# Performance work log

Measured on AMD Instinct MI355X. Metric: run time of the kernel, lower is better.

The kernel has to match this reference:

```python
import jax, jax.numpy as jnp
import numpy as np

DIMS = [2, 100, 100, 100, 98, 100, 100, 100, 100, 1]
BETA = 100.0

def _softplus100(x):
    # PyTorch Softplus(beta=100): (1/beta)*log(1+exp(beta*x)), linear above threshold 20
    bx = BETA * x
    return jnp.where(bx > 20.0, x, jax.nn.softplus(bx) / BETA)

def setup_inputs() -> dict:
    key = jax.random.key(0)
    keys = jax.random.split(key, 1 + 2 * 9)
    N = 1048576
    inp = {"input": jax.random.normal(keys[0], (N, 2), dtype=jnp.float32)}
    for l in range(9):
        in_dim = DIMS[l + 1] if l == 4 else DIMS[l]  # layer 4 is Linear(dims[5], dims[5]) = 100->100
        out_dim = DIMS[l + 1]
        # torch Linear convention: weight [out, in]
        scale = np.sqrt(2.0) / np.sqrt(out_dim)
        inp[f"W{l}"] = jax.random.normal(keys[1 + 2 * l], (out_dim, in_dim), dtype=jnp.float32) * scale
        inp[f"b{l}"] = jax.random.normal(keys[2 + 2 * l], (out_dim,), dtype=jnp.float32) * 0.01
    return inp

def reference(input, W0, b0, W1, b1, W2, b2, W3, b3, W4, b4, W5, b5, W6, b6, W7, b7, W8, b8):
    Ws = [W0, W1, W2, W3, W4, W5, W6, W7, W8]
    bs = [b0, b1, b2, b3, b4, b5, b6, b7, b8]
    x = input
    skip_input = input
    for l in range(9):
        if l == 4:
            x = jnp.concatenate([skip_input, x], axis=1)  # [N, 2+98] -> [N,100]
        x = x @ Ws[l].T + bs[l]
        if l < 8:
            x = _softplus100(x)
    return x  # [N, 1]
```

## Files before the change

### kernel.cpp

```cpp
#include <hip/hip_runtime.h>
#include <math.h>


typedef _Float16 half8 __attribute__((ext_vector_type(8)));
typedef _Float16 half4v __attribute__((ext_vector_type(4)));
typedef float f32x4 __attribute__((ext_vector_type(4)));

#define TPB 256
#define RPB 128

__device__ __forceinline__ float sp100(float x) {
    float t = __builtin_amdgcn_exp2f(-144.26950408889634f * fabsf(x));
    return fmaxf(x, 0.0f) + 0.0069314718055994531f * __builtin_amdgcn_logf(1.0f + t);
}

__device__ __forceinline__ int xhb(int m, int k) {
    return ((m << 8) + (k << 1)) ^ ((m & 7) << 4);
}

__global__ __launch_bounds__(TPB, 2) void mlp_fwd(
    const float* __restrict__ inp,
    const uint4* __restrict__ wpk,
    const float* __restrict__ W0, const float* __restrict__ b0,
    const float* __restrict__ W8, const float* __restrict__ b8,
    float* __restrict__ out)
{
    __shared__ _Float16 XH[RPB * 128];
    __shared__ _Float16 XL[RPB * 128];
    __shared__ float inps[RPB * 2];
    __shared__ float w0s[304];

    const int tid  = threadIdx.x;
    const int lane = tid & 63;
    const int wid  = tid >> 6;
    const int g    = lane >> 4;
    const int bid  = blockIdx.x;

    if (tid < RPB) {
        float2 v = *reinterpret_cast<const float2*>(inp + ((size_t)bid * RPB + tid) * 2);
        inps[tid * 2]     = v.x;
        inps[tid * 2 + 1] = v.y;
    }
    for (int q = tid; q < 304; q += TPB)
        w0s[q] = (q < 200) ? W0[q] : b0[q - 200];
    __syncthreads();

#pragma unroll
    for (int it = 0; it < 16; ++it) {
        int m = wid * 32 + it * 2 + (lane >> 5);
        int q = lane & 31;
        float i0 = inps[m * 2], i1 = inps[m * 2 + 1];
        half4v hh, hl;
#pragma unroll
        for (int p = 0; p < 4; ++p) {
            int c = q * 4 + p;
            float y = (c < 100)
                ? sp100(fmaf(i0, w0s[c * 2], fmaf(i1, w0s[c * 2 + 1], w0s[200 + c])))
                : ((c == 100) ? 1.0f : 0.0f);
            _Float16 h = (_Float16)y;
            hh[p] = h;
            hl[p] = (_Float16)(y - (float)h);
        }
        *reinterpret_cast<half4v*>(reinterpret_cast<char*>(XH) + xhb(m, q * 4)) = hh;
        *reinterpret_cast<half4v*>(reinterpret_cast<char*>(XL) + xhb(m, q * 4)) = hl;
    }

#pragma unroll 1
    for (int l = 1; l <= 7; ++l) {
        const uint4* __restrict__ wl = wpk + (size_t)(l - 1) * 3584;

        f32x4 acc[2][7];
#pragma unroll
        for (int rt = 0; rt < 2; ++rt)
#pragma unroll
            for (int t = 0; t < 7; ++t) acc[rt][t] = f32x4{0.f, 0.f, 0.f, 0.f};

#pragma unroll
        for (int s = 0; s < 4; ++s) {
            half8 Bh[2], Bl[2];
#pragma unroll
            for (int rt = 0; rt < 2; ++rt) {
                int m  = wid * 32 + rt * 16 + (lane & 15);
                int k0 = s * 32 + g * 8;
                Bh[rt] = *reinterpret_cast<const half8*>(
                             reinterpret_cast<const char*>(XH) + xhb(m, k0));
                Bl[rt] = *reinterpret_cast<const half8*>(
                             reinterpret_cast<const char*>(XL) + xhb(m, k0));
            }
#pragma unroll
            for (int t = 0; t < 7; ++t) {
                union { uint4 v; half8 h; } wh, wlo;
                wh.v  = wl[(s * 7 + t) * 64 + lane];
                wlo.v = wl[1792 + (s * 7 + t) * 64 + lane];
#pragma unroll
                for (int rt = 0; rt < 2; ++rt) {
                    acc[rt][t] = __builtin_amdgcn_mfma_f32_16x16x32_f16(wh.h,  Bh[rt], acc[rt][t], 0, 0, 0);
                    acc[rt][t] = __builtin_amdgcn_mfma_f32_16x16x32_f16(wh.h,  Bl[rt], acc[rt][t], 0, 0, 0);
                    acc[rt][t] = __builtin_amdgcn_mfma_f32_16x16x32_f16(wlo.h, Bh[rt], acc[rt][t], 0, 0, 0);
                }
            }
        }

        if (l < 7) {
            const int Nl = (l == 3) ? 98 : 100;
#pragma unroll
            for (int rt = 0; rt < 2; ++rt) {
                int m = wid * 32 + rt * 16 + (lane & 15);
#pragma unroll
                for (int t = 0; t < 7; ++t) {
                    half4v hh, hl;
#pragma unroll
                    for (int i = 0; i < 4; ++i) {
                        int n = 16 * t + 4 * g + i;
                        float y = (n < Nl) ? sp100(acc[rt][t][i])
                                           : ((n == Nl) ? 1.0f : 0.0f);
                        _Float16 h = (_Float16)y;
                        hh[i] = h;
                        hl[i] = (_Float16)(y - (float)h);
                    }
                    if (l != 3) {
                        *reinterpret_cast<half4v*>(
                            reinterpret_cast<char*>(XH) + xhb(m, 16 * t + 4 * g)) = hh;
                        *reinterpret_cast<half4v*>(
                            reinterpret_cast<char*>(XL) + xhb(m, 16 * t + 4 * g)) = hl;
                    } else {
#pragma unroll
                        for (int i = 0; i < 4; ++i) {
                            int c = 16 * t + 4 * g + i + 2;
                            *reinterpret_cast<_Float16*>(
                                reinterpret_cast<char*>(XH) + xhb(m, c)) = hh[i];
                            *reinterpret_cast<_Float16*>(
                                reinterpret_cast<char*>(XL) + xhb(m, c)) = hl[i];
                        }
                    }
                }
            }
            if (l == 3 && lane < 32) {
                int m = wid * 32 + lane;
#pragma unroll
                for (int c = 0; c < 2; ++c) {
                    float v = inps[m * 2 + c];
                    _Float16 h = (_Float16)v;
                    *reinterpret_cast<_Float16*>(
                        reinterpret_cast<char*>(XH) + xhb(m, c)) = h;
                    *reinterpret_cast<_Float16*>(
                        reinterpret_cast<char*>(XL) + xhb(m, c)) = (_Float16)(v - (float)h);
                }
            }
        } else {
            float w84[7][4];
#pragma unroll
            for (int t = 0; t < 6; ++t) {
                float4 w4 = *reinterpret_cast<const float4*>(W8 + 16 * t + 4 * g);
                w84[t][0] = w4.x; w84[t][1] = w4.y; w84[t][2] = w4.z; w84[t][3] = w4.w;
            }
#pragma unroll
            for (int i = 0; i < 4; ++i) {
                int n = 96 + 4 * g + i;
                w84[6][i] = (n < 100) ? W8[n] : 0.0f;
            }
            float p8[2] = {0.0f, 0.0f};
#pragma unroll
            for (int rt = 0; rt < 2; ++rt)
#pragma unroll
                for (int t = 0; t < 7; ++t)
#pragma unroll
                    for (int i = 0; i < 4; ++i)
                        p8[rt] = fmaf(w84[t][i], sp100(acc[rt][t][i]), p8[rt]);
            float b8v = b8[0];
#pragma unroll
            for (int rt = 0; rt < 2; ++rt) {
                float v = p8[rt];
                v += __shfl_xor(v, 16);
                v += __shfl_xor(v, 32);
                if (lane < 16)
                    out[(size_t)bid * RPB + wid * 32 + rt * 16 + lane] = v + b8v;
            }
        }
    }
}

__global__ void pack_weights(
    const float* __restrict__ W1, const float* __restrict__ W2,
    const float* __restrict__ W3, const float* __restrict__ W4,
    const float* __restrict__ W5, const float* __restrict__ W6,
    const float* __restrict__ W7,
    const float* __restrict__ b1, const float* __restrict__ b2,
    const float* __restrict__ b3, const float* __restrict__ b4,
    const float* __restrict__ b5, const float* __restrict__ b6,
    const float* __restrict__ b7,
    uint4* __restrict__ wpk)
{
    const float* Wt[7] = {W1, W2, W3, W4, W5, W6, W7};
    const float* Bt[7] = {b1, b2, b3, b4, b5, b6, b7};
    const float* W = Wt[blockIdx.x];
    const float* B = Bt[blockIdx.x];
    const int Nl = (blockIdx.x == 2) ? 98 : 100;
    for (int e = threadIdx.x; e < 3584; e += 256) {
        int term = e / 1792;
        int r    = e - term * 1792;
        int lane = r & 63;
        int st   = r >> 6;
        int s    = st / 7;
        int t    = st - s * 7;
        union { _Float16 h[8]; uint4 v; } pk;
#pragma unroll
        for (int jj = 0; jj < 8; ++jj) {
            int k = s * 32 + (lane >> 4) * 8 + jj;
            int n = t * 16 + (lane & 15);
            float val = 0.0f;
            if (n < Nl) {
                if (k < 100)       val = W[n * 100 + k];
                else if (k == 100) val = B[n];
            }
            _Float16 h = (_Float16)val;
            pk.h[jj] = term ? (_Float16)(val - (float)h) : h;
        }
        wpk[blockIdx.x * 3584 + term * 1792 + r] = pk.v;
    }
}

extern "C" void kernel_launch(void* const* d_in, const int* in_sizes, int n_in,
                              void* d_out, int out_size, void* d_ws, size_t ws_size,
                              hipStream_t stream)
{
    const float* inp = (const float*)d_in[0];
    const float* W[9];
    const float* B[9];
    for (int l = 0; l < 9; ++l) {
        W[l] = (const float*)d_in[1 + 2 * l];
        B[l] = (const float*)d_in[2 + 2 * l];
    }
    uint4* wpk = (uint4*)d_ws;
    float* out = (float*)d_out;
    const int N = in_sizes[0] / 2;

    pack_weights<<<7, 256, 0, stream>>>(W[1], W[2], W[3], W[4], W[5], W[6], W[7],
                                        B[1], B[2], B[3], B[4], B[5], B[6], B[7],
                                        wpk);
    mlp_fwd<<<N / RPB, TPB, 0, stream>>>(inp, wpk,
                                         W[0], B[0], W[8], B[8],
                                         out);
}
```

Baseline: 769.4 us.

## Double-buffer weight and activation fragments across K-steps and layers

Prefetches the next K-step's packed weight fragments (from global) and activation fragments (from LDS) into a second register buffer while the current step's MFMAs run. It also prefetches the next layer's first weight slice during the last step, and reorders the MFMAs so that independent accumulators are interleaved instead of chained three deep. The aim is to hide global and LDS load latency behind matrix work. The cost is many more live vector registers: two buffers of 14 weight half8 plus activations, on top of 14 accumulators. With launch bounds of 2 waves per SIMD, this risks spills or fewer resident waves.

After: 856.2 us. +11.3%, slower.

```diff
diff --git a/kernel.cpp b/kernel.cpp
--- a/kernel.cpp
+++ b/kernel.cpp
@@ -65,9 +65,28 @@
         *reinterpret_cast<half4v*>(reinterpret_cast<char*>(XL) + xhb(m, q * 4)) = hl;
     }
 
+    half8 wb[2][2][7];
+    half8 xb[2][2][2];
+
+    const half8* __restrict__ w8p = reinterpret_cast<const half8*>(wpk);
+
+#pragma unroll
+    for (int t = 0; t < 7; ++t) {
+        wb[0][0][t] = w8p[t * 64 + lane];
+        wb[0][1][t] = w8p[1792 + t * 64 + lane];
+    }
+#pragma unroll
+    for (int rt = 0; rt < 2; ++rt) {
+        int m = wid * 32 + rt * 16 + (lane & 15);
+        xb[0][0][rt] = *reinterpret_cast<const half8*>(
+                           reinterpret_cast<const char*>(XH) + xhb(m, g * 8));
+        xb[0][1][rt] = *reinterpret_cast<const half8*>(
+                           reinterpret_cast<const char*>(XL) + xhb(m, g * 8));
+    }
+
 #pragma unroll 1
     for (int l = 1; l <= 7; ++l) {
-        const uint4* __restrict__ wl = wpk + (size_t)(l - 1) * 3584;
+        const half8* __restrict__ wl = w8p + (size_t)(l - 1) * 3584;
 
         f32x4 acc[2][7];
 #pragma unroll
@@ -77,28 +96,50 @@
 
 #pragma unroll
         for (int s = 0; s < 4; ++s) {
-            half8 Bh[2], Bl[2];
-#pragma unroll
-            for (int rt = 0; rt < 2; ++rt) {
-                int m  = wid * 32 + rt * 16 + (lane & 15);
-                int k0 = s * 32 + g * 8;
-                Bh[rt] = *reinterpret_cast<const half8*>(
-                             reinterpret_cast<const char*>(XH) + xhb(m, k0));
-                Bl[rt] = *reinterpret_cast<const half8*>(
-                             reinterpret_cast<const char*>(XL) + xhb(m, k0));
-            }
-#pragma unroll
-            for (int t = 0; t < 7; ++t) {
-                union { uint4 v; half8 h; } wh, wlo;
-                wh.v  = wl[(s * 7 + t) * 64 + lane];
-                wlo.v = wl[1792 + (s * 7 + t) * 64 + lane];
+            const int cb = s & 1;
+            const int nb = cb ^ 1;
+
+            if (s < 3) {
+#pragma unroll
+                for (int t = 0; t < 7; ++t) {
+                    wb[nb][0][t] = wl[((s + 1) * 7 + t) * 64 + lane];
+                    wb[nb][1][t] = wl[1792 + ((s + 1) * 7 + t) * 64 + lane];
+                }
 #pragma unroll
                 for (int rt = 0; rt < 2; ++rt) {
-                    acc[rt][t] = __builtin_amdgcn_mfma_f32_16x16x32_f16(wh.h,  Bh[rt], acc[rt][t], 0, 0, 0);
-                    acc[rt][t] = __builtin_amdgcn_mfma_f32_16x16x32_f16(wh.h,  Bl[rt], acc[rt][t], 0, 0, 0);
-                    acc[rt][t] = __builtin_amdgcn_mfma_f32_16x16x32_f16(wlo.h, Bh[rt], acc[rt][t], 0, 0, 0);
-                }
-            }
+                    int m  = wid * 32 + rt * 16 + (lane & 15);
+                    int k0 = (s + 1) * 32 + g * 8;
+                    xb[nb][0][rt] = *reinterpret_cast<const half8*>(
+                                        reinterpret_cast<const char*>(XH) + xhb(m, k0));
+                    xb[nb][1][rt] = *reinterpret_cast<const half8*>(
+                                        reinterpret_cast<const char*>(XL) + xhb(m, k0));
+                }
+            } else if (l < 7) {
+#pragma unroll
+                for (int t = 0; t < 7; ++t) {
+                    wb[0][0][t] = wl[3584 + t * 64 + lane];
+                    wb[0][1][t] = wl[3584 + 1792 + t * 64 + lane];
+                }
+            }
+
+#pragma unroll
+            for (int t = 0; t < 7; ++t)
+#pragma unroll
+                for (int rt = 0; rt < 2; ++rt)
+                    acc[rt][t] = __builtin_amdgcn_mfma_f32_16x16x32_f16(
+                        wb[cb][0][t], xb[cb][0][rt], acc[rt][t], 0, 0, 0);
+#pragma unroll
+            for (int t = 0; t < 7; ++t)
+#pragma unroll
+                for (int rt = 0; rt < 2; ++rt)
+                    acc[rt][t] = __builtin_amdgcn_mfma_f32_16x16x32_f16(
+                        wb[cb][0][t], xb[cb][1][rt], acc[rt][t], 0, 0, 0);
+#pragma unroll
+            for (int t = 0; t < 7; ++t)
+#pragma unroll
+                for (int rt = 0; rt < 2; ++rt)
+                    acc[rt][t] = __builtin_amdgcn_mfma_f32_16x16x32_f16(
+                        wb[cb][1][t], xb[cb][0][rt], acc[rt][t], 0, 0, 0);
         }
 
         if (l < 7) {
@@ -146,6 +187,14 @@
                     *reinterpret_cast<_Float16*>(
                         reinterpret_cast<char*>(XL) + xhb(m, c)) = (_Float16)(v - (float)h);
                 }
+            }
+#pragma unroll
+            for (int rt = 0; rt < 2; ++rt) {
+                int m = wid * 32 + rt * 16 + (lane & 15);
+                xb[0][0][rt] = *reinterpret_cast<const half8*>(
+                                   reinterpret_cast<const char*>(XH) + xhb(m, g * 8));
+                xb[0][1][rt] = *reinterpret_cast<const half8*>(
+                                   reinterpret_cast<const char*>(XL) + xhb(m, g * 8));
             }
         } else {
             float w84[7][4];
```

## Double rows per block to reuse weight fragments across four row tiles

Applied to the files above, without the earlier changes.

Raises rows per block from 128 to 256, so each wave now computes four 16-row tiles and every weight fragment loaded from global memory feeds twice as many MFMAs. All seven weight hi/lo fragments for a k-step are loaded up front, and the MFMAs are grouped by precision term to give longer independent chains. Layer-0 weights move from shared memory into registers. In exchange, shared memory use doubles and the launch bound drops to one block per CU, which cuts occupancy and raises register pressure (112 accumulator registers per thread).

New measurement: 986.8 us. 28.3% more time.

```diff
diff --git a/kernel.cpp b/kernel.cpp
--- a/kernel.cpp
+++ b/kernel.cpp
@@ -7,7 +7,7 @@
 typedef float f32x4 __attribute__((ext_vector_type(4)));
 
 #define TPB 256
-#define RPB 128
+#define RPB 256
 
 __device__ __forceinline__ float sp100(float x) {
     float t = __builtin_amdgcn_exp2f(-144.26950408889634f * fabsf(x));
@@ -18,7 +18,7 @@
     return ((m << 8) + (k << 1)) ^ ((m & 7) << 4);
 }
 
-__global__ __launch_bounds__(TPB, 2) void mlp_fwd(
+__global__ __launch_bounds__(TPB, 1) void mlp_fwd(
     const float* __restrict__ inp,
     const uint4* __restrict__ wpk,
     const float* __restrict__ W0, const float* __restrict__ b0,
@@ -28,7 +28,6 @@
     __shared__ _Float16 XH[RPB * 128];
     __shared__ _Float16 XL[RPB * 128];
     __shared__ float inps[RPB * 2];
-    __shared__ float w0s[304];
 
     const int tid  = threadIdx.x;
     const int lane = tid & 63;
@@ -41,71 +40,93 @@
         inps[tid * 2]     = v.x;
         inps[tid * 2 + 1] = v.y;
     }
-    for (int q = tid; q < 304; q += TPB)
-        w0s[q] = (q < 200) ? W0[q] : b0[q - 200];
+
+    const int q = tid & 31;
+    float w00[4], w01[4], b0v[4];
+#pragma unroll
+    for (int p = 0; p < 4; ++p) {
+        int c = 4 * q + p;
+        if (c < 100) {
+            float2 w2 = *reinterpret_cast<const float2*>(W0 + 2 * c);
+            w00[p] = w2.x; w01[p] = w2.y; b0v[p] = b0[c];
+        } else { w00[p] = 0.f; w01[p] = 0.f; b0v[p] = 0.f; }
+    }
     __syncthreads();
 
-#pragma unroll
-    for (int it = 0; it < 16; ++it) {
-        int m = wid * 32 + it * 2 + (lane >> 5);
-        int q = lane & 31;
-        float i0 = inps[m * 2], i1 = inps[m * 2 + 1];
+#pragma unroll 4
+    for (int j = 0; j < 32; ++j) {
+        int r = (tid >> 5) + 8 * j;
+        float i0 = inps[r * 2], i1 = inps[r * 2 + 1];
         half4v hh, hl;
 #pragma unroll
         for (int p = 0; p < 4; ++p) {
-            int c = q * 4 + p;
+            int c = 4 * q + p;
             float y = (c < 100)
-                ? sp100(fmaf(i0, w0s[c * 2], fmaf(i1, w0s[c * 2 + 1], w0s[200 + c])))
+                ? sp100(fmaf(i0, w00[p], fmaf(i1, w01[p], b0v[p])))
                 : ((c == 100) ? 1.0f : 0.0f);
             _Float16 h = (_Float16)y;
             hh[p] = h;
             hl[p] = (_Float16)(y - (float)h);
         }
-        *reinterpret_cast<half4v*>(reinterpret_cast<char*>(XH) + xhb(m, q * 4)) = hh;
-        *reinterpret_cast<half4v*>(reinterpret_cast<char*>(XL) + xhb(m, q * 4)) = hl;
-    }
+        *reinterpret_cast<half4v*>(reinterpret_cast<char*>(XH) + xhb(r, 4 * q)) = hh;
+        *reinterpret_cast<half4v*>(reinterpret_cast<char*>(XL) + xhb(r, 4 * q)) = hl;
+    }
+
+    const half8* __restrict__ w8p = reinterpret_cast<const half8*>(wpk);
 
 #pragma unroll 1
     for (int l = 1; l <= 7; ++l) {
-        const uint4* __restrict__ wl = wpk + (size_t)(l - 1) * 3584;
-
-        f32x4 acc[2][7];
-#pragma unroll
-        for (int rt = 0; rt < 2; ++rt)
+        const half8* __restrict__ wl = w8p + (size_t)(l - 1) * 3584;
+
+        f32x4 acc[4][7];
+#pragma unroll
+        for (int rt = 0; rt < 4; ++rt)
 #pragma unroll
             for (int t = 0; t < 7; ++t) acc[rt][t] = f32x4{0.f, 0.f, 0.f, 0.f};
 
 #pragma unroll
         for (int s = 0; s < 4; ++s) {
-            half8 Bh[2], Bl[2];
-#pragma unroll
-            for (int rt = 0; rt < 2; ++rt) {
-                int m  = wid * 32 + rt * 16 + (lane & 15);
+            half8 xh[4], xl[4];
+#pragma unroll
+            for (int rt = 0; rt < 4; ++rt) {
+                int m  = wid * 64 + rt * 16 + (lane & 15);
                 int k0 = s * 32 + g * 8;
-                Bh[rt] = *reinterpret_cast<const half8*>(
+                xh[rt] = *reinterpret_cast<const half8*>(
                              reinterpret_cast<const char*>(XH) + xhb(m, k0));
-                Bl[rt] = *reinterpret_cast<const half8*>(
+                xl[rt] = *reinterpret_cast<const half8*>(
                              reinterpret_cast<const char*>(XL) + xhb(m, k0));
             }
+            half8 wh[7], wlo[7];
 #pragma unroll
             for (int t = 0; t < 7; ++t) {
-                union { uint4 v; half8 h; } wh, wlo;
-                wh.v  = wl[(s * 7 + t) * 64 + lane];
-                wlo.v = wl[1792 + (s * 7 + t) * 64 + lane];
-#pragma unroll
-                for (int rt = 0; rt < 2; ++rt) {
-                    acc[rt][t] = __builtin_amdgcn_mfma_f32_16x16x32_f16(wh.h,  Bh[rt], acc[rt][t], 0, 0, 0);
-                    acc[rt][t] = __builtin_amdgcn_mfma_f32_16x16x32_f16(wh.h,  Bl[rt], acc[rt][t], 0, 0, 0);
-                    acc[rt][t] = __builtin_amdgcn_mfma_f32_16x16x32_f16(wlo.h, Bh[rt], acc[rt][t], 0, 0, 0);
-                }
-            }
+                wh[t]  = wl[(s * 7 + t) * 64 + lane];
+                wlo[t] = wl[1792 + (s * 7 + t) * 64 + lane];
+            }
+#pragma unroll
+            for (int t = 0; t < 7; ++t)
+#pragma unroll
+                for (int rt = 0; rt < 4; ++rt)
+                    acc[rt][t] = __builtin_amdgcn_mfma_f32_16x16x32_f16(
+                        wh[t], xh[rt], acc[rt][t], 0, 0, 0);
+#pragma unroll
+            for (int t = 0; t < 7; ++t)
+#pragma unroll
+                for (int rt = 0; rt < 4; ++rt)
+                    acc[rt][t] = __builtin_amdgcn_mfma_f32_16x16x32_f16(
+                        wh[t], xl[rt], acc[rt][t], 0, 0, 0);
+#pragma unroll
+            for (int t = 0; t < 7; ++t)
+#pragma unroll
+                for (int rt = 0; rt < 4; ++rt)
+                    acc[rt][t] = __builtin_amdgcn_mfma_f32_16x16x32_f16(
+                        wlo[t], xh[rt], acc[rt][t], 0, 0, 0);
         }
 
         if (l < 7) {
             const int Nl = (l == 3) ? 98 : 100;
 #pragma unroll
-            for (int rt = 0; rt < 2; ++rt) {
-                int m = wid * 32 + rt * 16 + (lane & 15);
+            for (int rt = 0; rt < 4; ++rt) {
+                int m = wid * 64 + rt * 16 + (lane & 15);
 #pragma unroll
                 for (int t = 0; t < 7; ++t) {
                     half4v hh, hl;
@@ -135,8 +156,8 @@
                     }
                 }
             }
-            if (l == 3 && lane < 32) {
-                int m = wid * 32 + lane;
+            if (l == 3) {
+                int m = wid * 64 + lane;
 #pragma unroll
                 for (int c = 0; c < 2; ++c) {
                     float v = inps[m * 2 + c];
@@ -159,22 +180,19 @@
                 int n = 96 + 4 * g + i;
                 w84[6][i] = (n < 100) ? W8[n] : 0.0f;
             }
-            float p8[2] = {0.0f, 0.0f};
-#pragma unroll
-            for (int rt = 0; rt < 2; ++rt)
+            float b8v = b8[0];
+#pragma unroll
+            for (int rt = 0; rt < 4; ++rt) {
+                float p8 = 0.0f;
 #pragma unroll
                 for (int t = 0; t < 7; ++t)
 #pragma unroll
                     for (int i = 0; i < 4; ++i)
-                        p8[rt] = fmaf(w84[t][i], sp100(acc[rt][t][i]), p8[rt]);
-            float b8v = b8[0];
-#pragma unroll
-            for (int rt = 0; rt < 2; ++rt) {
-                float v = p8[rt];
-                v += __shfl_xor(v, 16);
-                v += __shfl_xor(v, 32);
+                        p8 = fmaf(w84[t][i], sp100(acc[rt][t][i]), p8);
+                p8 += __shfl_xor(p8, 16);
+                p8 += __shfl_xor(p8, 32);
                 if (lane < 16)
-                    out[(size_t)bid * RPB + wid * 32 + rt * 16 + lane] = v + b8v;
+                    out[(size_t)bid * RPB + wid * 64 + rt * 16 + lane] = p8 + b8v;
             }
         }
     }
```
